# Kernel optimization log

Hardware: AMD Instinct MI355X
Metric: run time of the kernel (lower is better)

The kernel has to match this reference:

```python
import jax, jax.numpy as jnp
import numpy as np

N_HEAD = 12
NUM_BLOCK_TOKENS = 64
SSMAX_S_INIT = 0.43


def setup_inputs() -> dict:
    key = jax.random.key(0)
    k1, k2, k3 = jax.random.split(key, 3)
    B, T, C = 2, 2048, 768
    x = jax.random.normal(k1, (B, T, C), dtype=jnp.float32)
    # torch Linear weights: y = x @ W.T ; init scaled for stability
    c_attn_w = jax.random.normal(k2, (3 * C, C), dtype=jnp.float32) * 0.02
    c_proj_w = jax.random.normal(k3, (C, C), dtype=jnp.float32) * 0.02
    s = jnp.full((1,), SSMAX_S_INIT, dtype=jnp.float32)  # learnable SSMax scale
    return {"x": x, "c_attn_w": c_attn_w, "c_proj_w": c_proj_w, "s": s}


def reference(x, c_attn_w, c_proj_w, s):
    B, T, C = x.shape
    H, hd, n = N_HEAD, C // N_HEAD, NUM_BLOCK_TOKENS
    qkv = x @ c_attn_w.T                              # [B,T,3C]
    q, k, v = jnp.split(qkv, 3, axis=-1)
    q = q.reshape(B, T, H, hd).transpose(0, 2, 1, 3)  # [B,H,T,hd]
    k = k.reshape(B, T, H, hd).transpose(0, 2, 1, 3)
    v = v.reshape(B, T, H, hd).transpose(0, 2, 1, 3)
    att = jnp.einsum('bhqd,bhkd->bhqk', q, k) * (1.0 / np.sqrt(hd))
    # slot-based block mask reduces to block-causal: allow s_idx//n <= t_idx//n
    blk = jnp.arange(T) // n
    mask = blk[:, None] >= blk[None, :]               # [T,T] bool, True=attend
    scale = s[0] * np.log(T).astype(np.float32)       # SSMax: s * log(N)
    att = jnp.where(mask[None, None], att * scale, -jnp.inf)
    att = jax.nn.softmax(att, axis=-1)
    y = jnp.einsum('bhqk,bhkd->bhqd', att, v)
    y = y.transpose(0, 2, 1, 3).reshape(B, T, C)
    return y @ c_proj_w.T
```

## Files before the change

kernel.cpp:

```cpp
#include <hip/hip_runtime.h>
#include <hip/hip_bf16.h>
#include <stdint.h>

#define T_SEQ 2048
#define C_DIM 768
#define NH 12
#define HD 64
#define QK_LD 1536

typedef __attribute__((ext_vector_type(8))) short short8;
typedef __attribute__((ext_vector_type(4))) float f32x4;
typedef const __attribute__((address_space(1))) void* gas_ptr;
typedef __attribute__((address_space(3))) void* las_ptr;

static __device__ __forceinline__ unsigned short f2bf(float f) {
  union { float f; unsigned u; } c; c.f = f;
  unsigned u = c.u + 0x7fffu + ((c.u >> 16) & 1u);
  return (unsigned short)(u >> 16);
}

__global__ void cast3_kernel(const float* __restrict__ a, int na4,
                             const float* __restrict__ b, int nb4,
                             const float* __restrict__ c, int nc4,
                             unsigned short* __restrict__ oa,
                             unsigned short* __restrict__ ob,
                             unsigned short* __restrict__ oc) {
  int i = blockIdx.x * blockDim.x + threadIdx.x;
  int stride = gridDim.x * blockDim.x;
  int total = na4 + nb4 + nc4;
  for (; i < total; i += stride) {
    const float4* src; ushort4* dst; int j;
    if (i < na4)            { src = (const float4*)a; dst = (ushort4*)oa; j = i; }
    else if (i < na4 + nb4) { src = (const float4*)b; dst = (ushort4*)ob; j = i - na4; }
    else                    { src = (const float4*)c; dst = (ushort4*)oc; j = i - na4 - nb4; }
    float4 v = src[j];
    ushort4 o;
    o.x = f2bf(v.x); o.y = f2bf(v.y); o.z = f2bf(v.z); o.w = f2bf(v.w);
    dst[j] = o;
  }
}

template <int NP>
__device__ __forceinline__ void stage_tile(const unsigned short* g, int ld,
                                           unsigned short* ldsbase, int tid) {
#pragma unroll
  for (int p = 0; p < NP; ++p) {
    int j = p * 256 + tid;
    int row = j >> 2, cc = (j & 3) << 3;
    const unsigned short* ga = g + (size_t)row * ld + cc;
    unsigned short* la = ldsbase + p * 2048 + (tid >> 6) * 512;
    __builtin_amdgcn_global_load_lds((gas_ptr)ga, (las_ptr)la, 16, 0, 0);
  }
}

template <int BM, int EPI, int NY, int PERX>
__launch_bounds__(256, EPI == 0 ? 3 : 4)
__global__ void gemm_bt(const unsigned short* __restrict__ A,
                        const unsigned short* __restrict__ B,
                        int K,
                        unsigned short* __restrict__ obf,
                        unsigned short* __restrict__ vt,
                        float* __restrict__ ofp,
                        const float* __restrict__ sptr) {
  constexpr int MI = BM / 32;
  constexpr int ABUF = BM * 32;
  constexpr int BUF = ABUF + 4096;
  constexpr int LDS_SH = 2 * BUF;
  constexpr int TR_SH = (EPI == 0) ? 128 * 130 : 0;
  constexpr int TOT = LDS_SH > TR_SH ? LDS_SH : TR_SH;
  __shared__ __attribute__((aligned(16))) unsigned short smem[TOT];
  int tid = threadIdx.x;
  int lane = tid & 63, wave = tid >> 6;
  int L = blockIdx.x;
  int t0 = (L & 7) * PERX + (L >> 3);
  int row0 = (t0 / NY) * BM, col0 = (t0 % NY) * 128;
  int wr = (wave >> 1) * (BM / 2), wc = (wave & 1) * 64;
  int la = lane & 15, lb = lane >> 4;
  f32x4 acc[MI][4] = {};

  const unsigned short* Abase = A + (size_t)row0 * K;
  const unsigned short* Bbase = B + (size_t)col0 * K;
  stage_tile<BM / 64>(Abase, K, smem, tid);
  stage_tile<2>(Bbase, K, smem + ABUF, tid);
  __syncthreads();
  int cur = 0;
  int nt = K >> 5;
  for (int t = 0; t < nt; ++t) {
    if (t + 1 < nt) {
      stage_tile<BM / 64>(Abase + (t + 1) * 32, K, smem + (cur ^ 1) * BUF, tid);
      stage_tile<2>(Bbase + (t + 1) * 32, K, smem + (cur ^ 1) * BUF + ABUF, tid);
    }
    unsigned short* lds = smem + cur * BUF;
    short8 af[MI], bfr[4];
#pragma unroll
    for (int i = 0; i < MI; ++i)
      af[i] = *(const short8*)&lds[(wr + i * 16 + la) * 32 + lb * 8];
#pragma unroll
    for (int j = 0; j < 4; ++j)
      bfr[j] = *(const short8*)&lds[ABUF + (wc + j * 16 + la) * 32 + lb * 8];
#pragma unroll
    for (int i = 0; i < MI; ++i)
#pragma unroll
      for (int j = 0; j < 4; ++j)
        acc[i][j] = __builtin_amdgcn_mfma_f32_16x16x32_bf16(af[i], bfr[j], acc[i][j], 0, 0, 0);
    __syncthreads();
    cur ^= 1;
  }

  if (EPI == 0 && col0 >= 1536) {
#pragma unroll
    for (int i = 0; i < MI; ++i)
#pragma unroll
      for (int j = 0; j < 4; ++j)
#pragma unroll
        for (int r = 0; r < 4; ++r)
          smem[(wr + i * 16 + lb * 4 + r) * 130 + (wc + j * 16 + la)] =
              f2bf(acc[i][j][r]);
    __syncthreads();
    int bb = row0 >> 11, t0r = row0 & 2047;
    int cl = tid >> 1, half = tid & 1;
    int vcol = col0 - 1536 + cl;
    int h = vcol >> 6, d = vcol & 63;
    unsigned short* dst =
        vt + ((size_t)(bb * NH + h) * 64 + d) * T_SEQ + t0r + half * 64;
#pragma unroll
    for (int j = 0; j < 8; ++j) {
      short8 v8;
#pragma unroll
      for (int e = 0; e < 8; ++e)
        v8[e] = (short)smem[(half * 64 + j * 8 + e) * 130 + cl];
      *(short8*)(dst + j * 8) = v8;
    }
    return;
  }

  float qs = 0.f;
  if (EPI == 0)
    qs = sptr[0] * 7.624618986159398f  * 0.125f
         * 1.4426950408889634f ;
#pragma unroll
  for (int i = 0; i < MI; ++i) {
    int gr0 = row0 + wr + i * 16 + lb * 4;
#pragma unroll
    for (int j = 0; j < 4; ++j) {
      int gc = col0 + wc + j * 16 + la;
#pragma unroll
      for (int r = 0; r < 4; ++r) {
        float v = acc[i][j][r];
        int rr = gr0 + r;
        if (EPI == 0) {
          obf[(size_t)rr * QK_LD + gc] = f2bf(gc < 768 ? v * qs : v);
        } else {
          ofp[(size_t)rr * C_DIM + gc] = v;
        }
      }
    }
  }
}

__device__ __forceinline__ void attn_stage(const unsigned short* kg,
                                           const unsigned short* vg,
                                           char* kbuf, int wave, int lane) {
  int l3 = lane >> 3;
  int cg = ((lane & 7) ^ l3) << 4;
#pragma unroll
  for (int q = 0; q < 2; ++q) {
    int rk = q * 32 + wave * 8 + l3;
    const unsigned short* ka = kg + (size_t)rk * QK_LD + (cg >> 1);
    char* kl = kbuf + (q * 32 + wave * 8) * 128;
    __builtin_amdgcn_global_load_lds((gas_ptr)ka, (las_ptr)kl, 16, 0, 0);
    const unsigned short* va = vg + (size_t)rk * T_SEQ + (cg >> 1);
    char* vl = kbuf + 8192 + (q * 32 + wave * 8) * 128;
    __builtin_amdgcn_global_load_lds((gas_ptr)va, (las_ptr)vl, 16, 0, 0);
  }
}

__launch_bounds__(256, 4)
__global__ void attn_kernel(const unsigned short* __restrict__ qkb,
                            const unsigned short* __restrict__ vt,
                            float* __restrict__ yp,
                            float* __restrict__ lsp,
                            unsigned short* __restrict__ yb) {
  __shared__ __attribute__((aligned(16))) char smem[2 * 16384 + 8192];

  int tid = threadIdx.x, lane = tid & 63, wave = tid >> 6;
  int la = lane & 15, lb = lane >> 4;
  int L = blockIdx.x;
  int ixcd = L >> 3;
  int bh = (L & 7) * 3 + ixcd / 48;
  int xx = 47 - (ixcd % 48);
  int qi, cch;
  if (xx < 16) { qi = xx; cch = 0; }
  else         { int t = xx - 16; qi = 16 + (t >> 1); cch = t & 1; }
  int kt0 = cch * 16;
  int kt1 = min(qi, kt0 + 15);
  int b = bh / NH, h = bh - b * NH;

  const unsigned short* qbase =
      qkb + ((size_t)(b * T_SEQ + qi * 64 + wave * 16 + la)) * QK_LD + h * HD;
  short8 qf0 = *(const short8*)(qbase + lb * 8);
  short8 qf1 = *(const short8*)(qbase + 32 + lb * 8);
  asm volatile("" :: "v"(qf0), "v"(qf1));

  f32x4 y[4] = {};
  float ls[4] = {0.f, 0.f, 0.f, 0.f};

  const unsigned short* kg0 = qkb + (size_t)b * T_SEQ * QK_LD + 768 + h * HD;
  const unsigned short* vg0 = vt + (size_t)bh * 64 * T_SEQ;
  char* pw = smem + 32768 + wave * 2048;

  attn_stage(kg0 + (size_t)kt0 * 64 * QK_LD, vg0 + kt0 * 64, smem, wave, lane);
  int cur = 0;

  for (int kt = kt0; kt <= kt1; ++kt) {
    asm volatile("" ::: "memory");
    __builtin_amdgcn_s_barrier();
    if (kt < kt1) {
      attn_stage(kg0 + (size_t)(kt + 1) * 64 * QK_LD, vg0 + (kt + 1) * 64,
                 smem + ((cur ^ 1) * 16384), wave, lane);
      asm volatile("s_waitcnt vmcnt(4)" ::: "memory");
    } else {
      asm volatile("s_waitcnt vmcnt(0)" ::: "memory");
    }
    __builtin_amdgcn_s_barrier();
    asm volatile("" ::: "memory");
    __builtin_amdgcn_sched_barrier(0);

    char* kl = smem + cur * 16384;
    char* vl = kl + 8192;

    f32x4 s[4] = {};
    __builtin_amdgcn_s_setprio(1);
#pragma unroll
    for (int fk = 0; fk < 4; ++fk) {
      int row = fk * 16 + la;
      {
        int off = (row * 128 + 0 * 64 + lb * 16) ^ ((row & 7) << 4);
        short8 kf = *(const short8*)(kl + off);
        s[fk] = __builtin_amdgcn_mfma_f32_16x16x32_bf16(qf0, kf, s[fk], 0, 0, 0);
      }
      {
        int off = (row * 128 + 1 * 64 + lb * 16) ^ ((row & 7) << 4);
        short8 kf = *(const short8*)(kl + off);
        s[fk] = __builtin_amdgcn_mfma_f32_16x16x32_bf16(qf1, kf, s[fk], 0, 0, 0);
      }
    }
    __builtin_amdgcn_s_setprio(0);

#pragma unroll
    for (int fk = 0; fk < 4; ++fk)
#pragma unroll
      for (int r = 0; r < 4; ++r) {
        float p = __builtin_amdgcn_exp2f(s[fk][r]);
        s[fk][r] = p;
        ls[r] += p;
        int row = lb * 4 + r;
        int off = (row * 128 + (fk * 16 + la) * 2) ^ ((row & 7) << 4);
        *(unsigned short*)(pw + off) = f2bf(p);
      }

    short8 pa[2];
#pragma unroll
    for (int ch = 0; ch < 2; ++ch) {
      int off = (la * 128 + ch * 64 + lb * 16) ^ ((la & 7) << 4);
      pa[ch] = *(const short8*)(pw + off);
    }
    __builtin_amdgcn_s_setprio(1);
#pragma unroll
    for (int fd = 0; fd < 4; ++fd) {
      int row = fd * 16 + la;
#pragma unroll
      for (int ch = 0; ch < 2; ++ch) {
        int off = (row * 128 + ch * 64 + lb * 16) ^ ((row & 7) << 4);
        short8 vf = *(const short8*)(vl + off);
        y[fd] = __builtin_amdgcn_mfma_f32_16x16x32_bf16(pa[ch], vf, y[fd], 0, 0, 0);
      }
    }
    __builtin_amdgcn_s_setprio(0);

    cur ^= 1;
  }

#pragma unroll
  for (int r = 0; r < 4; ++r) {
    float v = ls[r];
    v += __shfl_xor(v, 1); v += __shfl_xor(v, 2);
    v += __shfl_xor(v, 4); v += __shfl_xor(v, 8);
    ls[r] = v;
  }
  int trow = qi * 64 + wave * 16 + lb * 4;

  if (qi < 16) {
    float inv[4];
#pragma unroll
    for (int r = 0; r < 4; ++r) inv[r] = 1.0f / ls[r];
#pragma unroll
    for (int fd = 0; fd < 4; ++fd)
#pragma unroll
      for (int r = 0; r < 4; ++r) {
        int rowg = b * T_SEQ + trow + r;
        int colg = h * HD + fd * 16 + la;
        yb[(size_t)rowg * C_DIM + colg] = f2bf(y[fd][r] * inv[r]);
      }
  } else {
    size_t slotbase = (size_t)cch * (24 * 2048);
    if (la == 0) {
#pragma unroll
      for (int r = 0; r < 4; ++r)
        lsp[slotbase + (size_t)bh * 2048 + trow + r] = ls[r];
    }
    float* ydst = yp + (slotbase + (size_t)bh * 2048) * 64;
#pragma unroll
    for (int fd = 0; fd < 4; ++fd)
#pragma unroll
      for (int r = 0; r < 4; ++r)
        ydst[(size_t)(trow + r) * 64 + fd * 16 + la] = y[fd][r];
  }
}

__global__ void norm_kernel(const float* __restrict__ yp,
                            const float* __restrict__ lsp,
                            unsigned short* __restrict__ yb) {
  int gid = blockIdx.x * blockDim.x + threadIdx.x;
  int dq = gid & 15;
  int rloc = gid >> 4;
  int bh = rloc >> 10, t = 1024 + (rloc & 1023);
  int row = bh * 2048 + t;
  int b = bh / NH, h = bh - b * NH;
  float denom = lsp[row] + lsp[24 * 2048 + row];
  float inv = 1.0f / denom;
  float4 y0 = ((const float4*)yp)[row * 16 + dq];
  float4 y1 = ((const float4*)yp)[(24 * 2048 * 16) + row * 16 + dq];
  ushort4 o;
  o.x = f2bf((y0.x + y1.x) * inv);
  o.y = f2bf((y0.y + y1.y) * inv);
  o.z = f2bf((y0.z + y1.z) * inv);
  o.w = f2bf((y0.w + y1.w) * inv);
  ((ushort4*)yb)[(size_t)(b * T_SEQ + t) * 192 + h * 16 + dq] = o;
}

extern "C" void kernel_launch(void* const* d_in, const int* in_sizes, int n_in,
                              void* d_out, int out_size, void* d_ws, size_t ws_size,
                              hipStream_t stream) {
  const float* x = (const float*)d_in[0];
  const float* attn_w = (const float*)d_in[1];
  const float* proj_w = (const float*)d_in[2];
  const float* s = (const float*)d_in[3];
  float* out = (float*)d_out;

  char* ws = (char*)d_ws;
  unsigned short* xb  = (unsigned short*)(ws);
  unsigned short* wab = (unsigned short*)(ws + 6291456);
  unsigned short* wpb = (unsigned short*)(ws + 9830400);
  unsigned short* qkb = (unsigned short*)(ws + 11010048);
  unsigned short* vtb = (unsigned short*)(ws + 23592960);
  unsigned short* yb  = (unsigned short*)(ws + 29884416);
  float*          yp  = (float*)(ws + 36175872);
  float*          lsp = (float*)(ws + 61341696);

  cast3_kernel<<<2048, 256, 0, stream>>>(x, 3145728 / 4, attn_w, 1769472 / 4,
                                         proj_w, 589824 / 4, xb, wab, wpb);

  gemm_bt<128, 0, 18, 72><<<576, 256, 0, stream>>>(xb, wab, 768, qkb, vtb, nullptr, s);

  attn_kernel<<<1152, 256, 0, stream>>>(qkb, vtb, yp, lsp, yb);

  norm_kernel<<<1536, 256, 0, stream>>>(yp, lsp, yb);

  gemm_bt<64, 1, 6, 48><<<384, 256, 0, stream>>>(yb, wpb, 768, nullptr, nullptr, out, nullptr);
}
```

Baseline: 149.3 us.

## Widen QKV GEMM tile to 256 columns and overlap loads with explicit vmcnt waits

The GEMM kernel now takes the N-tile width as a template parameter. The QKV projection uses 128x256 tiles (288 blocks) for more operand reuse per block. The main loop drops the trailing __syncthreads and instead uses a leading barrier, issues the next tile's global-to-LDS loads, waits with s_waitcnt vmcnt for only the current tile, then barriers again, so the prefetch overlaps the MFMAs. The V-transpose epilogue runs in two passes over 128-column halves. In exchange, the larger tile raises register pressure and cuts occupancy to 2 blocks per SIMD set, and the grid of 288 blocks may underfill the 256 CUs.

```diff
diff --git a/kernel.cpp b/kernel.cpp
--- a/kernel.cpp
+++ b/kernel.cpp
@@ -53,8 +53,16 @@
   }
 }
 
-template <int BM, int EPI, int NY, int PERX>
-__launch_bounds__(256, EPI == 0 ? 3 : 4)
+template <int N>
+__device__ __forceinline__ void wait_vmcnt() {
+  if constexpr (N == 0) asm volatile("s_waitcnt vmcnt(0)" ::: "memory");
+  else if constexpr (N == 3) asm volatile("s_waitcnt vmcnt(3)" ::: "memory");
+  else if constexpr (N == 6) asm volatile("s_waitcnt vmcnt(6)" ::: "memory");
+  else static_assert(N == 0 || N == 3 || N == 6, "add vmcnt literal");
+}
+
+template <int BM, int BN, int EPI, int NY, int PERX, int MAXB>
+__launch_bounds__(256, MAXB)
 __global__ void gemm_bt(const unsigned short* __restrict__ A,
                         const unsigned short* __restrict__ B,
                         int K,
@@ -63,8 +71,11 @@
                         float* __restrict__ ofp,
                         const float* __restrict__ sptr) {
   constexpr int MI = BM / 32;
+  constexpr int NJ = BN / 32;
+  constexpr int NPA = BM / 64, NPB = BN / 64;
+  constexpr int S = NPA + NPB;
   constexpr int ABUF = BM * 32;
-  constexpr int BUF = ABUF + 4096;
+  constexpr int BUF = ABUF + BN * 32;
   constexpr int LDS_SH = 2 * BUF;
   constexpr int TR_SH = (EPI == 0) ? 128 * 130 : 0;
   constexpr int TOT = LDS_SH > TR_SH ? LDS_SH : TR_SH;
@@ -73,63 +84,77 @@
   int lane = tid & 63, wave = tid >> 6;
   int L = blockIdx.x;
   int t0 = (L & 7) * PERX + (L >> 3);
-  int row0 = (t0 / NY) * BM, col0 = (t0 % NY) * 128;
-  int wr = (wave >> 1) * (BM / 2), wc = (wave & 1) * 64;
+  int row0 = (t0 / NY) * BM, col0 = (t0 % NY) * BN;
+  int wr = (wave >> 1) * (BM / 2), wc = (wave & 1) * (BN / 2);
   int la = lane & 15, lb = lane >> 4;
-  f32x4 acc[MI][4] = {};
+  f32x4 acc[MI][NJ] = {};
 
   const unsigned short* Abase = A + (size_t)row0 * K;
   const unsigned short* Bbase = B + (size_t)col0 * K;
-  stage_tile<BM / 64>(Abase, K, smem, tid);
-  stage_tile<2>(Bbase, K, smem + ABUF, tid);
-  __syncthreads();
+  stage_tile<NPA>(Abase, K, smem, tid);
+  stage_tile<NPB>(Bbase, K, smem + ABUF, tid);
   int cur = 0;
   int nt = K >> 5;
   for (int t = 0; t < nt; ++t) {
+    asm volatile("" ::: "memory");
+    __builtin_amdgcn_s_barrier();
     if (t + 1 < nt) {
-      stage_tile<BM / 64>(Abase + (t + 1) * 32, K, smem + (cur ^ 1) * BUF, tid);
-      stage_tile<2>(Bbase + (t + 1) * 32, K, smem + (cur ^ 1) * BUF + ABUF, tid);
-    }
+      stage_tile<NPA>(Abase + (t + 1) * 32, K, smem + (cur ^ 1) * BUF, tid);
+      stage_tile<NPB>(Bbase + (t + 1) * 32, K, smem + (cur ^ 1) * BUF + ABUF, tid);
+      wait_vmcnt<S>();
+    } else {
+      wait_vmcnt<0>();
+    }
+    __builtin_amdgcn_s_barrier();
+    asm volatile("" ::: "memory");
+    __builtin_amdgcn_sched_barrier(0);
+
     unsigned short* lds = smem + cur * BUF;
-    short8 af[MI], bfr[4];
+    short8 af[MI], bfr[NJ];
 #pragma unroll
     for (int i = 0; i < MI; ++i)
       af[i] = *(const short8*)&lds[(wr + i * 16 + la) * 32 + lb * 8];
 #pragma unroll
-    for (int j = 0; j < 4; ++j)
+    for (int j = 0; j < NJ; ++j)
       bfr[j] = *(const short8*)&lds[ABUF + (wc + j * 16 + la) * 32 + lb * 8];
 #pragma unroll
     for (int i = 0; i < MI; ++i)
 #pragma unroll
-      for (int j = 0; j < 4; ++j)
+      for (int j = 0; j < NJ; ++j)
         acc[i][j] = __builtin_amdgcn_mfma_f32_16x16x32_bf16(af[i], bfr[j], acc[i][j], 0, 0, 0);
-    __syncthreads();
     cur ^= 1;
   }
 
   if (EPI == 0 && col0 >= 1536) {
-#pragma unroll
-    for (int i = 0; i < MI; ++i)
-#pragma unroll
-      for (int j = 0; j < 4; ++j)
-#pragma unroll
-        for (int r = 0; r < 4; ++r)
-          smem[(wr + i * 16 + lb * 4 + r) * 130 + (wc + j * 16 + la)] =
-              f2bf(acc[i][j][r]);
     __syncthreads();
     int bb = row0 >> 11, t0r = row0 & 2047;
     int cl = tid >> 1, half = tid & 1;
-    int vcol = col0 - 1536 + cl;
-    int h = vcol >> 6, d = vcol & 63;
-    unsigned short* dst =
-        vt + ((size_t)(bb * NH + h) * 64 + d) * T_SEQ + t0r + half * 64;
-#pragma unroll
-    for (int j = 0; j < 8; ++j) {
-      short8 v8;
-#pragma unroll
-      for (int e = 0; e < 8; ++e)
-        v8[e] = (short)smem[(half * 64 + j * 8 + e) * 130 + cl];
-      *(short8*)(dst + j * 8) = v8;
+#pragma unroll
+    for (int p = 0; p < BN / 128; ++p) {
+      if ((wave & 1) == p) {
+#pragma unroll
+        for (int i = 0; i < MI; ++i)
+#pragma unroll
+          for (int j = 0; j < NJ; ++j)
+#pragma unroll
+            for (int r = 0; r < 4; ++r)
+              smem[(wr + i * 16 + lb * 4 + r) * 130 + (j * 16 + la)] =
+                  f2bf(acc[i][j][r]);
+      }
+      __syncthreads();
+      int vcol = col0 - 1536 + p * 128 + cl;
+      int h = vcol >> 6, d = vcol & 63;
+      unsigned short* dst =
+          vt + ((size_t)(bb * NH + h) * 64 + d) * T_SEQ + t0r + half * 64;
+#pragma unroll
+      for (int j = 0; j < 8; ++j) {
+        short8 v8;
+#pragma unroll
+        for (int e = 0; e < 8; ++e)
+          v8[e] = (short)smem[(half * 64 + j * 8 + e) * 130 + cl];
+        *(short8*)(dst + j * 8) = v8;
+      }
+      __syncthreads();
     }
     return;
   }
@@ -142,7 +167,7 @@
   for (int i = 0; i < MI; ++i) {
     int gr0 = row0 + wr + i * 16 + lb * 4;
 #pragma unroll
-    for (int j = 0; j < 4; ++j) {
+    for (int j = 0; j < NJ; ++j) {
       int gc = col0 + wc + j * 16 + la;
 #pragma unroll
       for (int r = 0; r < 4; ++r) {
@@ -361,11 +386,11 @@
   cast3_kernel<<<2048, 256, 0, stream>>>(x, 3145728 / 4, attn_w, 1769472 / 4,
                                          proj_w, 589824 / 4, xb, wab, wpb);
 
-  gemm_bt<128, 0, 18, 72><<<576, 256, 0, stream>>>(xb, wab, 768, qkb, vtb, nullptr, s);
+  gemm_bt<128, 256, 0, 9, 36, 2><<<288, 256, 0, stream>>>(xb, wab, 768, qkb, vtb, nullptr, s);
 
   attn_kernel<<<1152, 256, 0, stream>>>(qkb, vtb, yp, lsp, yb);
 
   norm_kernel<<<1536, 256, 0, stream>>>(yp, lsp, yb);
 
-  gemm_bt<64, 1, 6, 48><<<384, 256, 0, stream>>>(yb, wpb, 768, nullptr, nullptr, out, nullptr);
-}
+  gemm_bt<64, 128, 1, 6, 48, 4><<<384, 256, 0, stream>>>(yb, wpb, 768, nullptr, nullptr, out, nullptr);
+}
```

After: 149.8 us. No clear change (+0.4%).

## Fuse x cast into QKV GEMM and split-K combine into projection GEMM

Applied to the files above, without the earlier changes.

Drops the separate bf16 cast of x: the QKV GEMM now loads fp32 x and packs it to bf16 with v_cvt_pk_bf16_f32 while staging into LDS. The norm kernel is removed too, so the projection GEMM reads the two attention partial outputs and log-sum terms and normalizes them inline for the second half of rows. GEMM column tiles shrink from 128 to 96, which raises block counts to 768 and 512. This saves two launches and an intermediate round trip, but the A staging becomes synchronous register loads instead of async global_load_lds, and the fp32 A reads are repeated for every column tile.

```diff
diff --git a/kernel.cpp b/kernel.cpp
--- a/kernel.cpp
+++ b/kernel.cpp
@@ -19,20 +19,29 @@
   return (unsigned short)(u >> 16);
 }
 
-__global__ void cast3_kernel(const float* __restrict__ a, int na4,
+static __device__ __forceinline__ unsigned cvtpk(float lo, float hi) {
+  unsigned r;
+  asm("v_cvt_pk_bf16_f32 %0, %1, %2" : "=v"(r) : "v"(lo), "v"(hi));
+  return r;
+}
+static __device__ __forceinline__ short8 pack8(float4 a, float4 b) {
+  union { unsigned u[4]; short8 s; } r;
+  r.u[0] = cvtpk(a.x, a.y); r.u[1] = cvtpk(a.z, a.w);
+  r.u[2] = cvtpk(b.x, b.y); r.u[3] = cvtpk(b.z, b.w);
+  return r.s;
+}
+
+__global__ void castw_kernel(const float* __restrict__ a, int na4,
                              const float* __restrict__ b, int nb4,
-                             const float* __restrict__ c, int nc4,
                              unsigned short* __restrict__ oa,
-                             unsigned short* __restrict__ ob,
-                             unsigned short* __restrict__ oc) {
+                             unsigned short* __restrict__ ob) {
   int i = blockIdx.x * blockDim.x + threadIdx.x;
   int stride = gridDim.x * blockDim.x;
-  int total = na4 + nb4 + nc4;
+  int total = na4 + nb4;
   for (; i < total; i += stride) {
     const float4* src; ushort4* dst; int j;
-    if (i < na4)            { src = (const float4*)a; dst = (ushort4*)oa; j = i; }
-    else if (i < na4 + nb4) { src = (const float4*)b; dst = (ushort4*)ob; j = i - na4; }
-    else                    { src = (const float4*)c; dst = (ushort4*)oc; j = i - na4 - nb4; }
+    if (i < na4) { src = (const float4*)a; dst = (ushort4*)oa; j = i; }
+    else         { src = (const float4*)b; dst = (ushort4*)ob; j = i - na4; }
     float4 v = src[j];
     ushort4 o;
     o.x = f2bf(v.x); o.y = f2bf(v.y); o.z = f2bf(v.z); o.w = f2bf(v.w);
@@ -40,68 +49,114 @@
   }
 }
 
-template <int NP>
-__device__ __forceinline__ void stage_tile(const unsigned short* g, int ld,
-                                           unsigned short* ldsbase, int tid) {
-#pragma unroll
-  for (int p = 0; p < NP; ++p) {
-    int j = p * 256 + tid;
-    int row = j >> 2, cc = (j & 3) << 3;
-    const unsigned short* ga = g + (size_t)row * ld + cc;
-    unsigned short* la = ldsbase + p * 2048 + (tid >> 6) * 512;
-    __builtin_amdgcn_global_load_lds((gas_ptr)ga, (las_ptr)la, 16, 0, 0);
-  }
-}
-
-template <int BM, int EPI, int NY, int PERX>
-__launch_bounds__(256, EPI == 0 ? 3 : 4)
-__global__ void gemm_bt(const unsigned short* __restrict__ A,
-                        const unsigned short* __restrict__ B,
-                        int K,
-                        unsigned short* __restrict__ obf,
-                        unsigned short* __restrict__ vt,
-                        float* __restrict__ ofp,
-                        const float* __restrict__ sptr) {
+__device__ __forceinline__ void stage_b96(const unsigned short* g, int ld,
+                                          unsigned short* ldsb, int tid) {
+  {
+    int c = tid, row = c >> 2, col = (c & 3) << 3;
+    __builtin_amdgcn_global_load_lds((gas_ptr)(g + (size_t)row * ld + col),
+                                     (las_ptr)(ldsb + (tid >> 6) * 512), 16, 0, 0);
+  }
+  if (tid < 128) {
+    int c = 256 + tid, row = c >> 2, col = (c & 3) << 3;
+    __builtin_amdgcn_global_load_lds((gas_ptr)(g + (size_t)row * ld + col),
+                                     (las_ptr)(ldsb + 2048 + (tid >> 6) * 512), 16, 0, 0);
+  }
+}
+
+template <int BM, int EPI, int NY, int PERX, int MAXB>
+__launch_bounds__(256, MAXB)
+__global__ void gemm_fused(const float* __restrict__ Af,
+                           const unsigned short* __restrict__ Bw,
+                           const unsigned short* __restrict__ ybA,
+                           const float* __restrict__ yp,
+                           const float* __restrict__ lsp,
+                           unsigned short* __restrict__ obf,
+                           unsigned short* __restrict__ vt,
+                           float* __restrict__ ofp,
+                           const float* __restrict__ sptr) {
+  constexpr int K = 768;
   constexpr int MI = BM / 32;
   constexpr int ABUF = BM * 32;
-  constexpr int BUF = ABUF + 4096;
+  constexpr int BUF = ABUF + 96 * 32;
   constexpr int LDS_SH = 2 * BUF;
-  constexpr int TR_SH = (EPI == 0) ? 128 * 130 : 0;
+  constexpr int TR_SH = (EPI == 0) ? 128 * 98 : 0;
   constexpr int TOT = LDS_SH > TR_SH ? LDS_SH : TR_SH;
   __shared__ __attribute__((aligned(16))) unsigned short smem[TOT];
   int tid = threadIdx.x;
   int lane = tid & 63, wave = tid >> 6;
   int L = blockIdx.x;
   int t0 = (L & 7) * PERX + (L >> 3);
-  int row0 = (t0 / NY) * BM, col0 = (t0 % NY) * 128;
-  int wr = (wave >> 1) * (BM / 2), wc = (wave & 1) * 64;
+  int row0 = (t0 / NY) * BM, col0 = (t0 % NY) * 96;
+  int wr = (wave >> 1) * (BM / 2), wc = (wave & 1) * 48;
   int la = lane & 15, lb = lane >> 4;
-  f32x4 acc[MI][4] = {};
-
-  const unsigned short* Abase = A + (size_t)row0 * K;
-  const unsigned short* Bbase = B + (size_t)col0 * K;
-  stage_tile<BM / 64>(Abase, K, smem, tid);
-  stage_tile<2>(Bbase, K, smem + ABUF, tid);
+  f32x4 acc[MI][3] = {};
+
+  int arow = tid >> 2, acol = (tid & 3) << 3;
+  bool combine = (EPI == 1) && ((row0 & 2047) >= 1024);
+  const float* y0p = nullptr; const float* l0p = nullptr;
+  if (EPI == 1 && combine) {
+    int bb = row0 >> 11, trow = (row0 & 2047) + arow;
+    y0p = yp + ((size_t)(bb * NH) * 2048 + trow) * 64;
+    l0p = lsp + (size_t)(bb * NH) * 2048 + trow;
+  }
+
+  auto stage_a = [&](int k, unsigned short* lds) {
+    if constexpr (EPI == 0) {
+      const float* ab = Af + (size_t)(row0 + arow) * K + k + acol;
+      float4 a0 = *(const float4*)ab;
+      float4 a1 = *(const float4*)(ab + 4);
+      float4 a2 = *(const float4*)(ab + (size_t)64 * K);
+      float4 a3 = *(const float4*)(ab + (size_t)64 * K + 4);
+      unsigned short* d0 = &lds[arow * 32 + acol];
+      *(short8*)d0 = pack8(a0, a1);
+      *(short8*)(d0 + 64 * 32) = pack8(a2, a3);
+    } else if (!combine) {
+      const unsigned short* g = ybA + (size_t)(row0 + arow) * C_DIM + k + acol;
+      __builtin_amdgcn_global_load_lds((gas_ptr)g,
+                                       (las_ptr)(lds + (tid >> 6) * 512), 16, 0, 0);
+    } else {
+      int h = k >> 6;
+      int d0c = (k & 63) + acol;
+      const float* yr = y0p + (size_t)h * 2048 * 64 + d0c;
+      float4 y00 = *(const float4*)yr;
+      float4 y01 = *(const float4*)(yr + 4);
+      const float* yr1 = yr + (size_t)24 * 2048 * 64;
+      float4 y10 = *(const float4*)yr1;
+      float4 y11 = *(const float4*)(yr1 + 4);
+      const float* lr = l0p + (size_t)h * 2048;
+      float inv = 1.0f / (lr[0] + lr[24 * 2048]);
+      float4 s0, s1;
+      s0.x = (y00.x + y10.x) * inv; s0.y = (y00.y + y10.y) * inv;
+      s0.z = (y00.z + y10.z) * inv; s0.w = (y00.w + y10.w) * inv;
+      s1.x = (y01.x + y11.x) * inv; s1.y = (y01.y + y11.y) * inv;
+      s1.z = (y01.z + y11.z) * inv; s1.w = (y01.w + y11.w) * inv;
+      *(short8*)&lds[arow * 32 + acol] = pack8(s0, s1);
+    }
+  };
+
+  stage_a(0, smem);
+  stage_b96(Bw + (size_t)col0 * K, K, smem + ABUF, tid);
   __syncthreads();
   int cur = 0;
-  int nt = K >> 5;
+  constexpr int nt = K / 32;
   for (int t = 0; t < nt; ++t) {
     if (t + 1 < nt) {
-      stage_tile<BM / 64>(Abase + (t + 1) * 32, K, smem + (cur ^ 1) * BUF, tid);
-      stage_tile<2>(Bbase + (t + 1) * 32, K, smem + (cur ^ 1) * BUF + ABUF, tid);
+      stage_a((t + 1) * 32, smem + (cur ^ 1) * BUF);
+      stage_b96(Bw + (size_t)col0 * K + (t + 1) * 32, K,
+                smem + (cur ^ 1) * BUF + ABUF, tid);
     }
     unsigned short* lds = smem + cur * BUF;
-    short8 af[MI], bfr[4];
+    short8 af[MI], bfr[3];
 #pragma unroll
     for (int i = 0; i < MI; ++i)
       af[i] = *(const short8*)&lds[(wr + i * 16 + la) * 32 + lb * 8];
 #pragma unroll
-    for (int j = 0; j < 4; ++j)
+    for (int j = 0; j < 3; ++j)
       bfr[j] = *(const short8*)&lds[ABUF + (wc + j * 16 + la) * 32 + lb * 8];
 #pragma unroll
     for (int i = 0; i < MI; ++i)
 #pragma unroll
-      for (int j = 0; j < 4; ++j)
+      for (int j = 0; j < 3; ++j)
         acc[i][j] = __builtin_amdgcn_mfma_f32_16x16x32_bf16(af[i], bfr[j], acc[i][j], 0, 0, 0);
     __syncthreads();
     cur ^= 1;
@@ -111,25 +166,27 @@
 #pragma unroll
     for (int i = 0; i < MI; ++i)
 #pragma unroll
-      for (int j = 0; j < 4; ++j)
+      for (int j = 0; j < 3; ++j)
 #pragma unroll
         for (int r = 0; r < 4; ++r)
-          smem[(wr + i * 16 + lb * 4 + r) * 130 + (wc + j * 16 + la)] =
+          smem[(wr + i * 16 + lb * 4 + r) * 98 + (wc + j * 16 + la)] =
               f2bf(acc[i][j][r]);
     __syncthreads();
-    int bb = row0 >> 11, t0r = row0 & 2047;
-    int cl = tid >> 1, half = tid & 1;
-    int vcol = col0 - 1536 + cl;
-    int h = vcol >> 6, d = vcol & 63;
-    unsigned short* dst =
-        vt + ((size_t)(bb * NH + h) * 64 + d) * T_SEQ + t0r + half * 64;
-#pragma unroll
-    for (int j = 0; j < 8; ++j) {
-      short8 v8;
-#pragma unroll
-      for (int e = 0; e < 8; ++e)
-        v8[e] = (short)smem[(half * 64 + j * 8 + e) * 130 + cl];
-      *(short8*)(dst + j * 8) = v8;
+    if (tid < 192) {
+      int bb = row0 >> 11, t0r = row0 & 2047;
+      int cl = tid >> 1, half = tid & 1;
+      int vcol = col0 - 1536 + cl;
+      int h = vcol >> 6, d = vcol & 63;
+      unsigned short* dst =
+          vt + ((size_t)(bb * NH + h) * 64 + d) * T_SEQ + t0r + half * 64;
+#pragma unroll
+      for (int j = 0; j < 8; ++j) {
+        short8 v8;
+#pragma unroll
+        for (int e = 0; e < 8; ++e)
+          v8[e] = (short)smem[(half * 64 + j * 8 + e) * 98 + cl];
+        *(short8*)(dst + j * 8) = v8;
+      }
     }
     return;
   }
@@ -142,7 +199,7 @@
   for (int i = 0; i < MI; ++i) {
     int gr0 = row0 + wr + i * 16 + lb * 4;
 #pragma unroll
-    for (int j = 0; j < 4; ++j) {
+    for (int j = 0; j < 3; ++j) {
       int gc = col0 + wc + j * 16 + la;
 #pragma unroll
       for (int r = 0; r < 4; ++r) {
@@ -318,27 +375,6 @@
   }
 }
 
-__global__ void norm_kernel(const float* __restrict__ yp,
-                            const float* __restrict__ lsp,
-                            unsigned short* __restrict__ yb) {
-  int gid = blockIdx.x * blockDim.x + threadIdx.x;
-  int dq = gid & 15;
-  int rloc = gid >> 4;
-  int bh = rloc >> 10, t = 1024 + (rloc & 1023);
-  int row = bh * 2048 + t;
-  int b = bh / NH, h = bh - b * NH;
-  float denom = lsp[row] + lsp[24 * 2048 + row];
-  float inv = 1.0f / denom;
-  float4 y0 = ((const float4*)yp)[row * 16 + dq];
-  float4 y1 = ((const float4*)yp)[(24 * 2048 * 16) + row * 16 + dq];
-  ushort4 o;
-  o.x = f2bf((y0.x + y1.x) * inv);
-  o.y = f2bf((y0.y + y1.y) * inv);
-  o.z = f2bf((y0.z + y1.z) * inv);
-  o.w = f2bf((y0.w + y1.w) * inv);
-  ((ushort4*)yb)[(size_t)(b * T_SEQ + t) * 192 + h * 16 + dq] = o;
-}
-
 extern "C" void kernel_launch(void* const* d_in, const int* in_sizes, int n_in,
                               void* d_out, int out_size, void* d_ws, size_t ws_size,
                               hipStream_t stream) {
@@ -349,23 +385,22 @@
   float* out = (float*)d_out;
 
   char* ws = (char*)d_ws;
-  unsigned short* xb  = (unsigned short*)(ws);
-  unsigned short* wab = (unsigned short*)(ws + 6291456);
-  unsigned short* wpb = (unsigned short*)(ws + 9830400);
-  unsigned short* qkb = (unsigned short*)(ws + 11010048);
-  unsigned short* vtb = (unsigned short*)(ws + 23592960);
-  unsigned short* yb  = (unsigned short*)(ws + 29884416);
-  float*          yp  = (float*)(ws + 36175872);
-  float*          lsp = (float*)(ws + 61341696);
-
-  cast3_kernel<<<2048, 256, 0, stream>>>(x, 3145728 / 4, attn_w, 1769472 / 4,
-                                         proj_w, 589824 / 4, xb, wab, wpb);
-
-  gemm_bt<128, 0, 18, 72><<<576, 256, 0, stream>>>(xb, wab, 768, qkb, vtb, nullptr, s);
+  unsigned short* wab = (unsigned short*)(ws);
+  unsigned short* wpb = (unsigned short*)(ws + 3538944);
+  unsigned short* qkb = (unsigned short*)(ws + 4718592);
+  unsigned short* vtb = (unsigned short*)(ws + 17301504);
+  unsigned short* yb  = (unsigned short*)(ws + 23592960);
+  float*          yp  = (float*)(ws + 29884416);
+  float*          lsp = (float*)(ws + 55050240);
+
+  castw_kernel<<<512, 256, 0, stream>>>(attn_w, 1769472 / 4, proj_w, 589824 / 4,
+                                        wab, wpb);
+
+  gemm_fused<128, 0, 24, 96, 3><<<768, 256, 0, stream>>>(
+      x, wab, nullptr, nullptr, nullptr, qkb, vtb, nullptr, s);
 
   attn_kernel<<<1152, 256, 0, stream>>>(qkb, vtb, yp, lsp, yb);
 
-  norm_kernel<<<1536, 256, 0, stream>>>(yp, lsp, yb);
-
-  gemm_bt<64, 1, 6, 48><<<384, 256, 0, stream>>>(yb, wpb, 768, nullptr, nullptr, out, nullptr);
-}
+  gemm_fused<64, 1, 8, 64, 4><<<512, 256, 0, stream>>>(
+      nullptr, wpb, yb, yp, lsp, nullptr, nullptr, out, nullptr);
+}
```

After: 160.7 us. 7.7% more time.
